# Kernel tuning notes

Hardware: AMD Instinct MI355X
Metric: run time of the kernel (lower is better)

The kernel has to match this reference:

```python
import jax, jax.numpy as jnp
import numpy as np

B, N, C, H = 8, 1024, 1024, 16  # batch, seq, dim, heads
HID = 4 * C                     # mlp hidden (mlp_ratio=4.0)


def _ln(x, g, b, eps=1e-5):
    m = x.mean(-1, keepdims=True)
    v = ((x - m) ** 2).mean(-1, keepdims=True)
    return (x - m) / jnp.sqrt(v + eps) * g + b


def setup_inputs() -> dict:
    key = jax.random.key(0)
    ks = jax.random.split(key, 8)
    s = 0.02  # init scale
    f32 = jnp.float32
    return {
        "x": jax.random.normal(ks[0], (B, N, C), f32),
        "g1": jnp.ones((C,), f32), "b1": jnp.zeros((C,), f32),
        "Wq": jax.random.normal(ks[1], (C, C), f32) * s, "bq": jnp.zeros((C,), f32),
        "Wk": jax.random.normal(ks[2], (C, C), f32) * s, "bk": jnp.zeros((C,), f32),
        "Wv": jax.random.normal(ks[3], (C, C), f32) * s, "bv": jnp.zeros((C,), f32),
        "Wp": jax.random.normal(ks[4], (C, C), f32) * s, "bp": jnp.zeros((C,), f32),
        "g2": jnp.ones((C,), f32), "b2": jnp.zeros((C,), f32),
        "W1": jax.random.normal(ks[5], (C, HID), f32) * s, "c1": jnp.zeros((HID,), f32),
        "W2": jax.random.normal(ks[6], (HID, C), f32) * s, "c2": jnp.zeros((C,), f32),
    }


def reference(x, g1, b1, Wq, bq, Wk, bk, Wv, bv, Wp, bp, g2, b2, W1, c1, W2, c2):
    hd = C // H
    scale = hd ** -0.5
    # --- pre-norm self-attention ---
    h = _ln(x, g1, b1)
    # NOTE: faithful to source: direct reshape (B,N,C)->(B,H,N,hd), NOT the
    # standard reshape(B,N,H,hd).transpose -- the original code reshapes the
    # flat N*C block into H contiguous chunks of N*hd.
    q = (h @ Wq + bq).reshape(B, H, -1, hd)
    k = (h @ Wk + bk).reshape(B, H, -1, hd)
    v = (h @ Wv + bv).reshape(B, H, -1, hd)
    attn = jax.nn.softmax(jnp.einsum('bhnd,bhmd->bhnm', q, k) * scale, axis=-1)
    o = jnp.einsum('bhnm,bhmd->bhnd', attn, v)
    o = jnp.swapaxes(o, 1, 2).reshape(B, -1, C)  # (B,N,C)
    x = x + (o @ Wp + bp)
    # --- MLP block ---
    h2 = _ln(x, g2, b2)
    m = jax.nn.gelu(h2 @ W1 + c1, approximate=False) @ W2 + c2
    return x + m
```

## Files before the change

kernel.cpp:

```cpp
#include <hip/hip_runtime.h>
#include <hip/hip_bf16.h>
#include <math.h>

typedef __bf16 bf16_t;
typedef __bf16 bf16x4 __attribute__((ext_vector_type(4)));
typedef __bf16 bf16x8 __attribute__((ext_vector_type(8)));
typedef float  f32x4  __attribute__((ext_vector_type(4)));

typedef __attribute__((address_space(1))) const void GVoid;
typedef __attribute__((address_space(3))) void LVoid;

__device__ __forceinline__ void gld16(const void* g, void* l) {
    __builtin_amdgcn_global_load_lds((GVoid*)g, (LVoid*)l, 16, 0, 0);
}

__device__ __forceinline__ float gelu_exact(float v) {
    return 0.5f * v * (1.0f + erff(v * 0.7071067811865475f));
}

__global__ __launch_bounds__(256) void transpose_f32_bf16(
    const float* __restrict__ in, bf16_t* __restrict__ out,
    int R, int C, size_t inBatch, size_t outBatch)
{
    __shared__ bf16_t tile[64][65];
    const float* src = in  + (size_t)blockIdx.z * inBatch;
    bf16_t*      dst = out + (size_t)blockIdx.z * outBatch;
    const int r0 = blockIdx.y * 64, c0 = blockIdx.x * 64;
    const int t = threadIdx.x, tc = t & 63, tr = t >> 6;
#pragma unroll
    for (int i = 0; i < 16; ++i) {
        int r = tr + i * 4;
        tile[r][tc] = (bf16_t)src[(size_t)(r0 + r) * C + c0 + tc];
    }
    __syncthreads();
#pragma unroll
    for (int i = 0; i < 16; ++i) {
        int r = tr + i * 4;
        dst[(size_t)(c0 + r) * R + r0 + tc] = tile[tc][r];
    }
}

__global__ __launch_bounds__(256) void transpose_bf16(
    const bf16_t* __restrict__ in, bf16_t* __restrict__ out,
    int R, int C, size_t inBatch, size_t outBatch)
{
    __shared__ __align__(16) bf16_t tile[64][65];
    const bf16_t* src = in  + (size_t)blockIdx.z * inBatch;
    bf16_t*       dst = out + (size_t)blockIdx.z * outBatch;
    const int r0 = blockIdx.y * 64, c0 = blockIdx.x * 64;
    const int t = threadIdx.x, tc = t & 63, tr = t >> 6;
#pragma unroll
    for (int i = 0; i < 16; ++i) {
        int r = tr + i * 4;
        tile[r][tc] = src[(size_t)(r0 + r) * C + c0 + tc];
    }
    __syncthreads();
#pragma unroll
    for (int i = 0; i < 16; ++i) {
        int r = tr + i * 4;
        dst[(size_t)(c0 + r) * R + r0 + tc] = tile[tc][r];
    }
}

__global__ __launch_bounds__(256) void ln_kernel(
    const float* __restrict__ x, const float* __restrict__ g,
    const float* __restrict__ b, bf16_t* __restrict__ out)
{
    const int row = blockIdx.x, t = threadIdx.x;
    const float* xr = x + (size_t)row * 1024;
    float v[4];
#pragma unroll
    for (int i = 0; i < 4; ++i) v[i] = xr[t * 4 + i];
    float s = v[0] + v[1] + v[2] + v[3];
    float s2 = v[0]*v[0] + v[1]*v[1] + v[2]*v[2] + v[3]*v[3];
#pragma unroll
    for (int o = 1; o < 64; o <<= 1) { s += __shfl_xor(s, o); s2 += __shfl_xor(s2, o); }
    __shared__ float red[8];
    if ((t & 63) == 0) { red[t >> 6] = s; red[4 + (t >> 6)] = s2; }
    __syncthreads();
    s  = red[0] + red[1] + red[2] + red[3];
    s2 = red[4] + red[5] + red[6] + red[7];
    const float mean = s * (1.f / 1024.f);
    const float var  = fmaxf(s2 * (1.f / 1024.f) - mean * mean, 0.f);
    const float rstd = rsqrtf(var + 1e-5f);
#pragma unroll
    for (int i = 0; i < 4; ++i) {
        int c = t * 4 + i;
        out[(size_t)row * 1024 + c] =
            (bf16_t)((v[i] - mean) * rstd * g[c] + b[c]);
    }
}

template <int MODE>
__global__ __launch_bounds__(256) void gemm_bt(
    const bf16_t* __restrict__ A, const bf16_t* __restrict__ Bt,
    const float* __restrict__ bias, const float* resid_f,
    bf16_t* __restrict__ out_bf, float* out_f, int N, int K)
{
    __shared__ __align__(16) bf16_t As[128 * 32];
    __shared__ __align__(16) bf16_t Bs[128 * 32];
    const int t = threadIdx.x;
    const int wv = t >> 6, ln = t & 63;
    const int wx = wv & 1, wy = wv >> 1;
    const int l16 = ln & 15, quad = ln >> 4;
    const int m0 = blockIdx.x * 128, n0 = blockIdx.y * 128;

    f32x4 acc[4][4];
#pragma unroll
    for (int i = 0; i < 4; ++i)
#pragma unroll
        for (int j = 0; j < 4; ++j) acc[i][j] = f32x4{0.f, 0.f, 0.f, 0.f};

    const int arow = t >> 2;
    const int acol = (t & 3) << 3;
    const bf16_t* gA = A  + (size_t)(m0 + arow) * K + acol;
    const bf16_t* gB = Bt + (size_t)(n0 + arow) * K + acol;
    char* ldsA = (char*)As + wv * 1024;
    char* ldsB = (char*)Bs + wv * 1024;

    for (int kk = 0; kk < K; kk += 32) {
        __syncthreads();
        gld16(gA + kk,                 ldsA);
        gld16(gA + (size_t)64*K + kk,  ldsA + 4096);
        gld16(gB + kk,                 ldsB);
        gld16(gB + (size_t)64*K + kk,  ldsB + 4096);
        __syncthreads();

        bf16x8 af[4], bfr[4];
        const bf16_t* Ab = As + (wy * 64 + l16) * 32 + quad * 8;
        const bf16_t* Bb = Bs + (wx * 64 + l16) * 32 + quad * 8;
#pragma unroll
        for (int i = 0; i < 4; ++i) af[i]  = *(const bf16x8*)(Ab + i * 16 * 32);
#pragma unroll
        for (int j = 0; j < 4; ++j) bfr[j] = *(const bf16x8*)(Bb + j * 16 * 32);
#pragma unroll
        for (int i = 0; i < 4; ++i)
#pragma unroll
            for (int j = 0; j < 4; ++j)
                acc[i][j] = __builtin_amdgcn_mfma_f32_16x16x32_bf16(
                    af[i], bfr[j], acc[i][j], 0, 0, 0);
    }

#pragma unroll
    for (int i = 0; i < 4; ++i) {
        const int rowb = m0 + wy * 64 + i * 16 + quad * 4;
#pragma unroll
        for (int j = 0; j < 4; ++j) {
            const int col = n0 + wx * 64 + j * 16 + l16;
            const float bc = bias[col];
#pragma unroll
            for (int r = 0; r < 4; ++r) {
                const size_t idx = (size_t)(rowb + r) * N + col;
                float vv = acc[i][j][r] + bc;
                if (MODE == 1) out_f[idx] = vv + resid_f[idx];
                else if (MODE == 2) out_bf[idx] = (bf16_t)gelu_exact(vv);
                else out_f[idx] += acc[i][j][r];
            }
        }
    }
}

__global__ __launch_bounds__(256) void gemm_qkv(
    const bf16_t* __restrict__ A, const bf16_t* __restrict__ Bt,
    const float* __restrict__ bq, const float* __restrict__ bk,
    const float* __restrict__ bv,
    bf16_t* __restrict__ Qo, bf16_t* __restrict__ Ko, bf16_t* __restrict__ Vo,
    int K)
{
    __shared__ __align__(16) bf16_t As[128 * 32];
    __shared__ __align__(16) bf16_t Bs[128 * 32];
    const int t = threadIdx.x;
    const int wv = t >> 6, ln = t & 63;
    const int wx = wv & 1, wy = wv >> 1;
    const int l16 = ln & 15, quad = ln >> 4;
    const int m0 = blockIdx.x * 128, n0 = blockIdx.y * 128;

    f32x4 acc[4][4];
#pragma unroll
    for (int i = 0; i < 4; ++i)
#pragma unroll
        for (int j = 0; j < 4; ++j) acc[i][j] = f32x4{0.f, 0.f, 0.f, 0.f};

    const int arow = t >> 2;
    const int acol = (t & 3) << 3;
    const bf16_t* gA = A  + (size_t)(m0 + arow) * K + acol;
    const bf16_t* gB = Bt + (size_t)(n0 + arow) * K + acol;
    char* ldsA = (char*)As + wv * 1024;
    char* ldsB = (char*)Bs + wv * 1024;

    for (int kk = 0; kk < K; kk += 32) {
        __syncthreads();
        gld16(gA + kk,                 ldsA);
        gld16(gA + (size_t)64*K + kk,  ldsA + 4096);
        gld16(gB + kk,                 ldsB);
        gld16(gB + (size_t)64*K + kk,  ldsB + 4096);
        __syncthreads();

        bf16x8 af[4], bfr[4];
        const bf16_t* Ab = As + (wy * 64 + l16) * 32 + quad * 8;
        const bf16_t* Bb = Bs + (wx * 64 + l16) * 32 + quad * 8;
#pragma unroll
        for (int i = 0; i < 4; ++i) af[i]  = *(const bf16x8*)(Ab + i * 16 * 32);
#pragma unroll
        for (int j = 0; j < 4; ++j) bfr[j] = *(const bf16x8*)(Bb + j * 16 * 32);
#pragma unroll
        for (int i = 0; i < 4; ++i)
#pragma unroll
            for (int j = 0; j < 4; ++j)
                acc[i][j] = __builtin_amdgcn_mfma_f32_16x16x32_bf16(
                    af[i], bfr[j], acc[i][j], 0, 0, 0);
    }

    const int which = n0 >> 10;
    const float* bias = which == 0 ? bq : (which == 1 ? bk : bv);
    bf16_t* outp      = which == 0 ? Qo : (which == 1 ? Ko : Vo);
    const int nloc = n0 & 1023;
#pragma unroll
    for (int i = 0; i < 4; ++i) {
        const int rowb = m0 + wy * 64 + i * 16 + quad * 4;
#pragma unroll
        for (int j = 0; j < 4; ++j) {
            const int col = nloc + wx * 64 + j * 16 + l16;
            const float bc = bias[col];
#pragma unroll
            for (int r = 0; r < 4; ++r)
                outp[(size_t)(rowb + r) * 1024 + col] = (bf16_t)(acc[i][j][r] + bc);
        }
    }
}

__global__ __launch_bounds__(256, 2) void attn_kernel(
    const bf16_t* __restrict__ Q, const bf16_t* __restrict__ K,
    const bf16_t* __restrict__ Vt, bf16_t* __restrict__ O)
{
    __shared__ __align__(16) bf16_t smem[26112];
    bf16_t* Vs = smem;
    bf16_t* Ks = smem + 8704;
    bf16_t* Ps = smem + 8704;

    const int t = threadIdx.x;
    const int wv = t >> 6, ln = t & 63;
    const int l16 = ln & 15, quad = ln >> 4;
    const int qt = blockIdx.x, bh = blockIdx.y;
    const size_t hb = (size_t)bh << 16;

    bf16x8 qf[2][2];
#pragma unroll
    for (int rt = 0; rt < 2; ++rt)
#pragma unroll
        for (int ks = 0; ks < 2; ++ks)
            qf[rt][ks] = *(const bf16x8*)(Q + hb +
                (size_t)(qt*128 + wv*32 + rt*16 + l16) * 64 + ks*32 + quad*8);

    float m_run[2] = {-INFINITY, -INFINITY};
    float l_run[2] = {0.f, 0.f};
    f32x4 acc_o[2][4];
#pragma unroll
    for (int rt = 0; rt < 2; ++rt)
#pragma unroll
        for (int dt = 0; dt < 4; ++dt) acc_o[rt][dt] = f32x4{0.f, 0.f, 0.f, 0.f};

    const int krow = t >> 3, kcol = (t & 7) << 3;
    const int vrow = t >> 4, vcol = (t & 15) << 3;
    const float sc = 0.125f;

    for (int j = 0; j < 8; ++j) {
        bf16x8 kg[4], vg[4];
#pragma unroll
        for (int i = 0; i < 4; ++i) {
            kg[i] = *(const bf16x8*)(K  + hb + (size_t)(j*128 + i*32 + krow)*64 + kcol);
            vg[i] = *(const bf16x8*)(Vt + hb + (size_t)(i*16 + vrow)*1024 + j*128 + vcol);
        }
        __syncthreads();
#pragma unroll
        for (int i = 0; i < 4; ++i) {
            *(bf16x8*)(Ks + (i*32 + krow)*72 + kcol)  = kg[i];
            *(bf16x8*)(Vs + (i*16 + vrow)*136 + vcol) = vg[i];
        }
        __syncthreads();

        f32x4 accs[8][2];
#pragma unroll
        for (int nt = 0; nt < 8; ++nt)
#pragma unroll
            for (int rt = 0; rt < 2; ++rt) accs[nt][rt] = f32x4{0.f, 0.f, 0.f, 0.f};
#pragma unroll
        for (int ks = 0; ks < 2; ++ks)
#pragma unroll
            for (int nt = 0; nt < 8; ++nt) {
                bf16x8 kf = *(const bf16x8*)(Ks + (nt*16 + l16)*72 + ks*32 + quad*8);
#pragma unroll
                for (int rt = 0; rt < 2; ++rt)
                    accs[nt][rt] = __builtin_amdgcn_mfma_f32_16x16x32_bf16(
                        kf, qf[rt][ks], accs[nt][rt], 0, 0, 0);
            }

#pragma unroll
        for (int rt = 0; rt < 2; ++rt) {
            float mx = -INFINITY;
#pragma unroll
            for (int nt = 0; nt < 8; ++nt)
#pragma unroll
                for (int r = 0; r < 4; ++r) mx = fmaxf(mx, accs[nt][rt][r]);
            mx *= sc;
            mx = fmaxf(mx, __shfl_xor(mx, 16));
            mx = fmaxf(mx, __shfl_xor(mx, 32));
            const float mnew  = fmaxf(m_run[rt], mx);
            const float alpha = __expf(m_run[rt] - mnew);
            m_run[rt] = mnew;
            float rs = 0.f;
#pragma unroll
            for (int nt = 0; nt < 8; ++nt)
#pragma unroll
                for (int r = 0; r < 4; ++r) {
                    float p = __expf(accs[nt][rt][r] * sc - mnew);
                    accs[nt][rt][r] = p;
                    rs += p;
                }
            rs += __shfl_xor(rs, 16);
            rs += __shfl_xor(rs, 32);
            l_run[rt] = l_run[rt] * alpha + rs;
#pragma unroll
            for (int r = 0; r < 4; ++r) {
                const float af = __shfl(alpha, quad*4 + r, 16);
#pragma unroll
                for (int dt = 0; dt < 4; ++dt) acc_o[rt][dt][r] *= af;
            }
        }

        __syncthreads();
#pragma unroll
        for (int rt = 0; rt < 2; ++rt) {
            const int mrow = wv*32 + rt*16 + l16;
#pragma unroll
            for (int nt = 0; nt < 8; ++nt) {
                bf16x4 pk;
#pragma unroll
                for (int r = 0; r < 4; ++r) pk[r] = (bf16_t)accs[nt][rt][r];
                *(bf16x4*)(Ps + mrow*136 + nt*16 + quad*4) = pk;
            }
        }
#pragma unroll
        for (int ks = 0; ks < 4; ++ks) {
            bf16x8 ap[2];
#pragma unroll
            for (int rt = 0; rt < 2; ++rt)
                ap[rt] = *(const bf16x8*)(Ps + (wv*32 + rt*16 + l16)*136 + ks*32 + quad*8);
#pragma unroll
            for (int dt = 0; dt < 4; ++dt) {
                bf16x8 bvv = *(const bf16x8*)(Vs + (dt*16 + l16)*136 + ks*32 + quad*8);
#pragma unroll
                for (int rt = 0; rt < 2; ++rt)
                    acc_o[rt][dt] = __builtin_amdgcn_mfma_f32_16x16x32_bf16(
                        ap[rt], bvv, acc_o[rt][dt], 0, 0, 0);
            }
        }
    }

    const int b = bh >> 4, h = bh & 15;
#pragma unroll
    for (int rt = 0; rt < 2; ++rt) {
#pragma unroll
        for (int r = 0; r < 4; ++r) {
            const float inv = 1.f / __shfl(l_run[rt], quad*4 + r, 16);
            const int m = qt*128 + wv*32 + rt*16 + quad*4 + r;
#pragma unroll
            for (int dt = 0; dt < 4; ++dt) {
                const int d = dt*16 + l16;
                O[((size_t)b*1024 + m)*1024 + h*64 + d] =
                    (bf16_t)(acc_o[rt][dt][r] * inv);
            }
        }
    }
}

extern "C" void kernel_launch(void* const* d_in, const int* in_sizes, int n_in,
                              void* d_out, int out_size, void* d_ws, size_t ws_size,
                              hipStream_t stream)
{
    (void)in_sizes; (void)n_in;
    const size_t MB = 1ull << 20;
    if (ws_size < 64 * MB) {
        hipMemsetAsync(d_out, 0, (size_t)out_size * sizeof(float), stream);
        return;
    }

    const float* x  = (const float*)d_in[0];
    const float* g1 = (const float*)d_in[1];
    const float* b1 = (const float*)d_in[2];
    const float* Wq = (const float*)d_in[3];
    const float* bq = (const float*)d_in[4];
    const float* Wk = (const float*)d_in[5];
    const float* bk = (const float*)d_in[6];
    const float* Wv = (const float*)d_in[7];
    const float* bv = (const float*)d_in[8];
    const float* Wp = (const float*)d_in[9];
    const float* bp = (const float*)d_in[10];
    const float* g2 = (const float*)d_in[11];
    const float* b2 = (const float*)d_in[12];
    const float* W1 = (const float*)d_in[13];
    const float* c1 = (const float*)d_in[14];
    const float* W2 = (const float*)d_in[15];
    const float* c2 = (const float*)d_in[16];

    char* ws = (char*)d_ws;
    bf16_t* Kb  = (bf16_t*)(ws);
    bf16_t* Vb  = (bf16_t*)(ws + 16 * MB);
    bf16_t* Cs  = (bf16_t*)(ws + 32 * MB);
    bf16_t* WqT = (bf16_t*)(ws + 48 * MB);
    bf16_t* WpT = (bf16_t*)(ws + 54 * MB);
    bf16_t* W1T = (bf16_t*)(ws + 56 * MB);
    bf16_t* W2T = (bf16_t*)(ws + 48 * MB);
    bf16_t* Qb  = (bf16_t*)d_out;
    bf16_t* Ob  = Vb;
    bf16_t* hid = Kb;
    bf16_t* h2  = Cs;
    float*  x2  = (float*)d_out;
    float*  outf = (float*)d_out;

    const dim3 blk(256);

    transpose_f32_bf16<<<dim3(16, 16, 1), blk, 0, stream>>>(Wq, WqT,              1024, 1024, 0, 0);
    transpose_f32_bf16<<<dim3(16, 16, 1), blk, 0, stream>>>(Wk, WqT + 1024*1024,  1024, 1024, 0, 0);
    transpose_f32_bf16<<<dim3(16, 16, 1), blk, 0, stream>>>(Wv, WqT + 2*1024*1024, 1024, 1024, 0, 0);
    transpose_f32_bf16<<<dim3(16, 16, 1), blk, 0, stream>>>(Wp, WpT,              1024, 1024, 0, 0);
    transpose_f32_bf16<<<dim3(64, 16, 1), blk, 0, stream>>>(W1, W1T,              1024, 4096, 0, 0);

    ln_kernel<<<8192, blk, 0, stream>>>(x, g1, b1, Cs);

    gemm_qkv<<<dim3(64, 24), blk, 0, stream>>>(Cs, WqT, bq, bk, bv, Qb, Kb, Vb, 1024);

    transpose_bf16<<<dim3(1, 16, 128), blk, 0, stream>>>(Vb, Cs, 1024, 64, 65536, 65536);

    attn_kernel<<<dim3(8, 128), blk, 0, stream>>>(Qb, Kb, Cs, Ob);

    gemm_bt<1><<<dim3(64, 8), blk, 0, stream>>>(Ob, WpT, bp, x, nullptr, x2, 1024, 1024);

    transpose_f32_bf16<<<dim3(16, 32, 2), blk, 0, stream>>>(
        W2, W2T, 2048, 1024, 2048*1024, 2048*1024);

    ln_kernel<<<8192, blk, 0, stream>>>(x2, g2, b2, h2);

    for (int c = 0; c < 2; ++c) {
        gemm_bt<2><<<dim3(64, 16), blk, 0, stream>>>(
            h2, W1T + (size_t)c * 2048 * 1024, c1 + c * 2048, nullptr,
            hid, nullptr, 2048, 1024);
        if (c == 0)
            gemm_bt<1><<<dim3(64, 8), blk, 0, stream>>>(
                hid, W2T, c2, outf, nullptr, outf, 1024, 2048);
        else
            gemm_bt<5><<<dim3(64, 8), blk, 0, stream>>>(
                hid, W2T + (size_t)2048 * 1024, c2, nullptr, nullptr,
                outf, 1024, 2048);
    }
}
```

Before: 616.6 us.

## Use 32x32x16 MFMA in GEMMs, tanh-form GELU, batch weight transposes

Both GEMM kernels switch from 16x16x32 to 32x32x16 bf16 MFMA tiles with 2x2 accumulators per wave, cutting LDS fragment reads per MFMA and changing the epilogue row mapping. The exact erf-based GELU is replaced by a sigmoid form of the tanh approximation using __expf. Four separate weight-transpose launches are merged into one kernel indexed by blockIdx.z, trimming launch overhead. The GELU swap changes numerics slightly, which is an approximation risk against the exact reference.

```diff
diff --git a/kernel.cpp b/kernel.cpp
--- a/kernel.cpp
+++ b/kernel.cpp
@@ -6,6 +6,7 @@
 typedef __bf16 bf16x4 __attribute__((ext_vector_type(4)));
 typedef __bf16 bf16x8 __attribute__((ext_vector_type(8)));
 typedef float  f32x4  __attribute__((ext_vector_type(4)));
+typedef float  f32x16 __attribute__((ext_vector_type(16)));
 
 typedef __attribute__((address_space(1))) const void GVoid;
 typedef __attribute__((address_space(3))) void LVoid;
@@ -14,8 +15,36 @@
     __builtin_amdgcn_global_load_lds((GVoid*)g, (LVoid*)l, 16, 0, 0);
 }
 
-__device__ __forceinline__ float gelu_exact(float v) {
-    return 0.5f * v * (1.0f + erff(v * 0.7071067811865475f));
+__device__ __forceinline__ float gelu_fast(float x) {
+    float x2 = x * x;
+    float y  = fmaf(0.044715f * x2, x, x);
+    float e  = __expf(-1.5957691216057308f * y);
+    return x / (1.0f + e);
+}
+
+struct TP4 {
+    const float *s0, *s1, *s2, *s3;
+    bf16_t *d0, *d1, *d2, *d3;
+};
+__global__ __launch_bounds__(256) void transpose4_f32_bf16(TP4 p)
+{
+    __shared__ bf16_t tile[64][65];
+    const int z = blockIdx.z;
+    const float* src = z == 0 ? p.s0 : z == 1 ? p.s1 : z == 2 ? p.s2 : p.s3;
+    bf16_t*      dst = z == 0 ? p.d0 : z == 1 ? p.d1 : z == 2 ? p.d2 : p.d3;
+    const int r0 = blockIdx.y * 64, c0 = blockIdx.x * 64;
+    const int t = threadIdx.x, tc = t & 63, tr = t >> 6;
+#pragma unroll
+    for (int i = 0; i < 16; ++i) {
+        int r = tr + i * 4;
+        tile[r][tc] = (bf16_t)src[(size_t)(r0 + r) * 1024 + c0 + tc];
+    }
+    __syncthreads();
+#pragma unroll
+    for (int i = 0; i < 16; ++i) {
+        int r = tr + i * 4;
+        dst[(size_t)(c0 + r) * 1024 + r0 + tc] = tile[tc][r];
+    }
 }
 
 __global__ __launch_bounds__(256) void transpose_f32_bf16(
@@ -102,14 +131,16 @@
     const int t = threadIdx.x;
     const int wv = t >> 6, ln = t & 63;
     const int wx = wv & 1, wy = wv >> 1;
-    const int l16 = ln & 15, quad = ln >> 4;
+    const int l32 = ln & 31, half = ln >> 5;
     const int m0 = blockIdx.x * 128, n0 = blockIdx.y * 128;
 
-    f32x4 acc[4][4];
-#pragma unroll
-    for (int i = 0; i < 4; ++i)
-#pragma unroll
-        for (int j = 0; j < 4; ++j) acc[i][j] = f32x4{0.f, 0.f, 0.f, 0.f};
+    f32x16 acc[2][2];
+#pragma unroll
+    for (int i = 0; i < 2; ++i)
+#pragma unroll
+        for (int j = 0; j < 2; ++j)
+#pragma unroll
+            for (int r = 0; r < 16; ++r) acc[i][j][r] = 0.f;
 
     const int arow = t >> 2;
     const int acol = (t & 3) << 3;
@@ -126,34 +157,40 @@
         gld16(gB + (size_t)64*K + kk,  ldsB + 4096);
         __syncthreads();
 
-        bf16x8 af[4], bfr[4];
-        const bf16_t* Ab = As + (wy * 64 + l16) * 32 + quad * 8;
-        const bf16_t* Bb = Bs + (wx * 64 + l16) * 32 + quad * 8;
-#pragma unroll
-        for (int i = 0; i < 4; ++i) af[i]  = *(const bf16x8*)(Ab + i * 16 * 32);
-#pragma unroll
-        for (int j = 0; j < 4; ++j) bfr[j] = *(const bf16x8*)(Bb + j * 16 * 32);
-#pragma unroll
-        for (int i = 0; i < 4; ++i)
-#pragma unroll
-            for (int j = 0; j < 4; ++j)
-                acc[i][j] = __builtin_amdgcn_mfma_f32_16x16x32_bf16(
-                    af[i], bfr[j], acc[i][j], 0, 0, 0);
-    }
-
-#pragma unroll
-    for (int i = 0; i < 4; ++i) {
-        const int rowb = m0 + wy * 64 + i * 16 + quad * 4;
-#pragma unroll
-        for (int j = 0; j < 4; ++j) {
-            const int col = n0 + wx * 64 + j * 16 + l16;
-            const float bc = bias[col];
-#pragma unroll
-            for (int r = 0; r < 4; ++r) {
-                const size_t idx = (size_t)(rowb + r) * N + col;
+        bf16x8 af[2][2], bfr[2][2];
+        const bf16_t* Ab = As + (wy * 64 + l32) * 32 + half * 8;
+        const bf16_t* Bb = Bs + (wx * 64 + l32) * 32 + half * 8;
+#pragma unroll
+        for (int i = 0; i < 2; ++i)
+#pragma unroll
+            for (int kc = 0; kc < 2; ++kc) {
+                af[i][kc]  = *(const bf16x8*)(Ab + i * 1024 + kc * 16);
+                bfr[i][kc] = *(const bf16x8*)(Bb + i * 1024 + kc * 16);
+            }
+#pragma unroll
+        for (int kc = 0; kc < 2; ++kc)
+#pragma unroll
+            for (int i = 0; i < 2; ++i)
+#pragma unroll
+                for (int j = 0; j < 2; ++j)
+                    acc[i][j] = __builtin_amdgcn_mfma_f32_32x32x16_bf16(
+                        af[i][kc], bfr[j][kc], acc[i][j], 0, 0, 0);
+    }
+
+#pragma unroll
+    for (int j = 0; j < 2; ++j) {
+        const int col = n0 + wx * 64 + j * 32 + l32;
+        const float bc = bias[col];
+#pragma unroll
+        for (int i = 0; i < 2; ++i) {
+            const int rowb = m0 + wy * 64 + i * 32 + 4 * half;
+#pragma unroll
+            for (int r = 0; r < 16; ++r) {
+                const int row = rowb + (r & 3) + 8 * (r >> 2);
+                const size_t idx = (size_t)row * N + col;
                 float vv = acc[i][j][r] + bc;
                 if (MODE == 1) out_f[idx] = vv + resid_f[idx];
-                else if (MODE == 2) out_bf[idx] = (bf16_t)gelu_exact(vv);
+                else if (MODE == 2) out_bf[idx] = (bf16_t)gelu_fast(vv);
                 else out_f[idx] += acc[i][j][r];
             }
         }
@@ -172,14 +209,16 @@
     const int t = threadIdx.x;
     const int wv = t >> 6, ln = t & 63;
     const int wx = wv & 1, wy = wv >> 1;
-    const int l16 = ln & 15, quad = ln >> 4;
+    const int l32 = ln & 31, half = ln >> 5;
     const int m0 = blockIdx.x * 128, n0 = blockIdx.y * 128;
 
-    f32x4 acc[4][4];
-#pragma unroll
-    for (int i = 0; i < 4; ++i)
-#pragma unroll
-        for (int j = 0; j < 4; ++j) acc[i][j] = f32x4{0.f, 0.f, 0.f, 0.f};
+    f32x16 acc[2][2];
+#pragma unroll
+    for (int i = 0; i < 2; ++i)
+#pragma unroll
+        for (int j = 0; j < 2; ++j)
+#pragma unroll
+            for (int r = 0; r < 16; ++r) acc[i][j][r] = 0.f;
 
     const int arow = t >> 2;
     const int acol = (t & 3) << 3;
@@ -196,19 +235,24 @@
         gld16(gB + (size_t)64*K + kk,  ldsB + 4096);
         __syncthreads();
 
-        bf16x8 af[4], bfr[4];
-        const bf16_t* Ab = As + (wy * 64 + l16) * 32 + quad * 8;
-        const bf16_t* Bb = Bs + (wx * 64 + l16) * 32 + quad * 8;
-#pragma unroll
-        for (int i = 0; i < 4; ++i) af[i]  = *(const bf16x8*)(Ab + i * 16 * 32);
-#pragma unroll
-        for (int j = 0; j < 4; ++j) bfr[j] = *(const bf16x8*)(Bb + j * 16 * 32);
-#pragma unroll
-        for (int i = 0; i < 4; ++i)
-#pragma unroll
-            for (int j = 0; j < 4; ++j)
-                acc[i][j] = __builtin_amdgcn_mfma_f32_16x16x32_bf16(
-                    af[i], bfr[j], acc[i][j], 0, 0, 0);
+        bf16x8 af[2][2], bfr[2][2];
+        const bf16_t* Ab = As + (wy * 64 + l32) * 32 + half * 8;
+        const bf16_t* Bb = Bs + (wx * 64 + l32) * 32 + half * 8;
+#pragma unroll
+        for (int i = 0; i < 2; ++i)
+#pragma unroll
+            for (int kc = 0; kc < 2; ++kc) {
+                af[i][kc]  = *(const bf16x8*)(Ab + i * 1024 + kc * 16);
+                bfr[i][kc] = *(const bf16x8*)(Bb + i * 1024 + kc * 16);
+            }
+#pragma unroll
+        for (int kc = 0; kc < 2; ++kc)
+#pragma unroll
+            for (int i = 0; i < 2; ++i)
+#pragma unroll
+                for (int j = 0; j < 2; ++j)
+                    acc[i][j] = __builtin_amdgcn_mfma_f32_32x32x16_bf16(
+                        af[i][kc], bfr[j][kc], acc[i][j], 0, 0, 0);
     }
 
     const int which = n0 >> 10;
@@ -216,15 +260,17 @@
     bf16_t* outp      = which == 0 ? Qo : (which == 1 ? Ko : Vo);
     const int nloc = n0 & 1023;
 #pragma unroll
-    for (int i = 0; i < 4; ++i) {
-        const int rowb = m0 + wy * 64 + i * 16 + quad * 4;
-#pragma unroll
-        for (int j = 0; j < 4; ++j) {
-            const int col = nloc + wx * 64 + j * 16 + l16;
-            const float bc = bias[col];
-#pragma unroll
-            for (int r = 0; r < 4; ++r)
-                outp[(size_t)(rowb + r) * 1024 + col] = (bf16_t)(acc[i][j][r] + bc);
+    for (int j = 0; j < 2; ++j) {
+        const int col = nloc + wx * 64 + j * 32 + l32;
+        const float bc = bias[col];
+#pragma unroll
+        for (int i = 0; i < 2; ++i) {
+            const int rowb = m0 + wy * 64 + i * 32 + 4 * half;
+#pragma unroll
+            for (int r = 0; r < 16; ++r) {
+                const int row = rowb + (r & 3) + 8 * (r >> 2);
+                outp[(size_t)row * 1024 + col] = (bf16_t)(acc[i][j][r] + bc);
+            }
         }
     }
 }
@@ -420,11 +466,10 @@
 
     const dim3 blk(256);
 
-    transpose_f32_bf16<<<dim3(16, 16, 1), blk, 0, stream>>>(Wq, WqT,              1024, 1024, 0, 0);
-    transpose_f32_bf16<<<dim3(16, 16, 1), blk, 0, stream>>>(Wk, WqT + 1024*1024,  1024, 1024, 0, 0);
-    transpose_f32_bf16<<<dim3(16, 16, 1), blk, 0, stream>>>(Wv, WqT + 2*1024*1024, 1024, 1024, 0, 0);
-    transpose_f32_bf16<<<dim3(16, 16, 1), blk, 0, stream>>>(Wp, WpT,              1024, 1024, 0, 0);
-    transpose_f32_bf16<<<dim3(64, 16, 1), blk, 0, stream>>>(W1, W1T,              1024, 4096, 0, 0);
+    TP4 tp{Wq, Wk, Wv, Wp,
+           WqT, WqT + 1024*1024, WqT + 2*1024*1024, WpT};
+    transpose4_f32_bf16<<<dim3(16, 16, 4), blk, 0, stream>>>(tp);
+    transpose_f32_bf16<<<dim3(64, 16, 1), blk, 0, stream>>>(W1, W1T, 1024, 4096, 0, 0);
 
     ln_kernel<<<8192, blk, 0, stream>>>(x, g1, b1, Cs);
 
```

Measured after the change: 617.4 us. No clear change (+0.1%).
